# Optimization experiments

Hardware: AMD Instinct MI355X
Metric: run time of the kernel (lower is better)

The kernel has to match this reference:

```python
import jax, jax.numpy as jnp
import numpy as np

N_NODES = 100000


def gcn_conv(x, edge_index, W, b):
    # PyG GCNConv: add self-loops, symmetric normalization D^-1/2 (A+I) D^-1/2
    src, dst = edge_index[0], edge_index[1]
    n = x.shape[0]
    ones = jnp.ones(src.shape[0], dtype=x.dtype)
    deg = jax.ops.segment_sum(ones, dst, num_segments=n) + 1.0  # +1 self-loop
    dinv = jax.lax.rsqrt(deg)
    h = x @ W  # transform first (smaller gather traffic when out_dim < in_dim)
    norm = dinv[src] * dinv[dst]  # [E]
    msg = h[src] * norm[:, None]  # [E, out]
    agg = jax.ops.segment_sum(msg, dst, num_segments=n)
    agg = agg + h * (dinv * dinv)[:, None]  # self-loop contribution
    return agg + b


def setup_inputs() -> dict:
    key = jax.random.key(0)
    k = jax.random.split(key, 8)
    feature_size = 128
    n_edges = 3200000
    x = jax.random.normal(k[0], (N_NODES, feature_size), dtype=jnp.float32)
    edge_index = jax.random.randint(k[1], (2, n_edges), 0, N_NODES, dtype=jnp.int64)
    # Glorot-ish params
    W1 = jax.random.normal(k[2], (feature_size, 64), dtype=jnp.float32) / np.sqrt(feature_size)
    b1 = jnp.zeros((64,), dtype=jnp.float32)
    W2 = jax.random.normal(k[3], (64, 128), dtype=jnp.float32) / np.sqrt(64)
    b2 = jnp.zeros((128,), dtype=jnp.float32)
    Wfc = jax.random.normal(k[4], (128, 1), dtype=jnp.float32) / np.sqrt(128)
    bfc = jnp.zeros((1,), dtype=jnp.float32)
    return {"x": x, "edge_index": edge_index, "W1": W1, "b1": b1,
            "W2": W2, "b2": b2, "Wfc": Wfc, "bfc": bfc}


def reference(x, edge_index, W1, b1, W2, b2, Wfc, bfc):
    h = jax.nn.relu(gcn_conv(x, edge_index, W1, b1))
    h = jax.nn.relu(gcn_conv(h, edge_index, W2, b2))
    return h @ Wfc + bfc  # [N, 1]
```

## Files before the change

kernel.cpp:

```cpp
#include <hip/hip_runtime.h>
#include <hip/hip_fp16.h>

#define NN 100000
#define NBIN 128
#define RANGE 782
#define CAP 32768
#define CAPL 28672

__global__ __launch_bounds__(64) void k_detect(const unsigned int* ei, int* flag) {
    if (threadIdx.x == 0) {
        int is64 = 1;
        for (int i = 0; i < 64; ++i)
            if (ei[2 * i + 1] != 0u) { is64 = 0; break; }
        *flag = is64;
    }
}

__global__ __launch_bounds__(256) void k_binA(const int* __restrict__ ei_lo,
                                              const int* __restrict__ flag,
                                              int E, int* __restrict__ g_bincnt,
                                              unsigned* __restrict__ binbuf) {
    constexpr int ITER = 16;
    __shared__ int cnt[NBIN], basep[NBIN], pos[NBIN];
    const int t = threadIdx.x;
    const int base = blockIdx.x * (256 * ITER);
    const int s = (*flag) ? 2 : 1;
    unsigned pk[ITER];
    int bn[ITER];

    for (int i = t; i < NBIN; i += 256) { cnt[i] = 0; pos[i] = 0; }
    __syncthreads();

#pragma unroll
    for (int i = 0; i < ITER; ++i) {
        int e = base + i * 256 + t;
        if (e < E) {
            int src = __builtin_nontemporal_load(&ei_lo[(long long)s * e]);
            int dst = __builtin_nontemporal_load(&ei_lo[(long long)s * (E + e)]);
            int b = dst / RANGE;
            bn[i] = b;
            pk[i] = ((unsigned)(dst - b * RANGE) << 17) | (unsigned)src;
            atomicAdd(&cnt[b], 1);
        } else bn[i] = -1;
    }
    __syncthreads();
    for (int i = t; i < NBIN; i += 256)
        basep[i] = atomicAdd(&g_bincnt[i], cnt[i]);
    __syncthreads();
#pragma unroll
    for (int i = 0; i < ITER; ++i) {
        if (bn[i] >= 0) {
            int r = atomicAdd(&pos[bn[i]], 1);
            binbuf[(long long)bn[i] * CAP + basep[bn[i]] + r] = pk[i];
        }
    }
}

__global__ __launch_bounds__(512) void k_build(const unsigned* __restrict__ binbuf,
                                               const int* __restrict__ g_bincnt,
                                               int* __restrict__ row_ptr,
                                               float* __restrict__ dinv,
                                               int* __restrict__ csr, int n, int E) {
    __shared__ unsigned ebuf[CAPL];
    __shared__ int cnt[1024];
    __shared__ int ssum[512];
    __shared__ int pref[NBIN];
    const int t = threadIdx.x;
    const int bin = blockIdx.x;
    const int lo = bin * RANGE;
    const int rn = min(RANGE, n - lo);
    const int nE = min(g_bincnt[bin], CAPL);
    const unsigned* __restrict__ src = binbuf + (long long)bin * CAP;

    cnt[t] = 0; cnt[t + 512] = 0;
    if (t < NBIN) pref[t] = g_bincnt[t];
    __syncthreads();

    for (int i = t; i < nE; i += 512) {
        unsigned e = src[i];
        ebuf[i] = e;
        atomicAdd(&cnt[(int)(e >> 17)], 1);
    }
    __syncthreads();

    for (int off = 1; off < NBIN; off <<= 1) {
        int add = (t >= off && t < NBIN) ? pref[t - off] : 0;
        __syncthreads();
        if (t < NBIN) pref[t] += add;
        __syncthreads();
    }
    const int bstart = (bin > 0) ? pref[bin - 1] : 0;

    int a = cnt[2 * t], b = cnt[2 * t + 1];
    ssum[t] = a + b;
    __syncthreads();
    for (int off = 1; off < 512; off <<= 1) {
        int add = (t >= off) ? ssum[t - off] : 0;
        __syncthreads();
        ssum[t] += add;
        __syncthreads();
    }
    int prev = (t > 0) ? ssum[t - 1] : 0;
    cnt[2 * t] = prev;
    cnt[2 * t + 1] = prev + a;
    if (2 * t < rn) {
        row_ptr[lo + 2 * t] = bstart + prev;
        dinv[lo + 2 * t] = rsqrtf((float)a + 1.f);
    }
    if (2 * t + 1 < rn) {
        row_ptr[lo + 2 * t + 1] = bstart + prev + a;
        dinv[lo + 2 * t + 1] = rsqrtf((float)b + 1.f);
    }
    if (bin == NBIN - 1 && t == 0) row_ptr[n] = E;
    __syncthreads();

    for (int i = t; i < nE; i += 512) {
        unsigned e = ebuf[i];
        int slot = bstart + atomicAdd(&cnt[(int)(e >> 17)], 1);
        csr[slot] = (int)(e & 0x1FFFFu);
    }
}

__global__ __launch_bounds__(256) void k_gemm1(const float* __restrict__ X,
                                               const float* __restrict__ W,
                                               const float* __restrict__ dinv,
                                               __half* __restrict__ H, int n) {
    constexpr int K = 128, C = 64, RPT = 2;
    constexpr int CG = C / 4, RS = 256 / CG, RT = RS * RPT, XS = K + 4;
    __shared__ float Ws[K * C];
    __shared__ float Xs[RT * XS];
    const int t = threadIdx.x;

    for (int i = t * 4; i < K * C; i += 1024)
        *(float4*)&Ws[i] = *(const float4*)&W[i];

    const int row0 = blockIdx.x * RT;
    for (int i = t * 4; i < RT * K; i += 1024) {
        int r = i / K, k = i % K;
        int gr = row0 + r;
        float4 v = make_float4(0.f, 0.f, 0.f, 0.f);
        if (gr < n) v = *(const float4*)&X[(long long)gr * K + k];
        *(float4*)&Xs[r * XS + k] = v;
    }
    __syncthreads();

    const int cg = t % CG, rs = t / CG;
    float acc[RPT][4];
#pragma unroll
    for (int i = 0; i < RPT; ++i)
#pragma unroll
        for (int j = 0; j < 4; ++j) acc[i][j] = 0.f;

#pragma unroll 2
    for (int k4 = 0; k4 < K / 4; ++k4) {
        float4 xv[RPT];
#pragma unroll
        for (int i = 0; i < RPT; ++i)
            xv[i] = *(float4*)&Xs[(rs * RPT + i) * XS + k4 * 4];
#pragma unroll
        for (int j = 0; j < 4; ++j) {
            float4 w = *(float4*)&Ws[(k4 * 4 + j) * C + cg * 4];
#pragma unroll
            for (int i = 0; i < RPT; ++i) {
                float xvj = (&xv[i].x)[j];
                acc[i][0] = fmaf(xvj, w.x, acc[i][0]);
                acc[i][1] = fmaf(xvj, w.y, acc[i][1]);
                acc[i][2] = fmaf(xvj, w.z, acc[i][2]);
                acc[i][3] = fmaf(xvj, w.w, acc[i][3]);
            }
        }
    }
#pragma unroll
    for (int i = 0; i < RPT; ++i) {
        int gr = row0 + rs * RPT + i;
        if (gr < n) {
            float sc = dinv[gr];
            union { __half h[4]; uint2 u; } pk;
            pk.h[0] = __float2half(acc[i][0] * sc);
            pk.h[1] = __float2half(acc[i][1] * sc);
            pk.h[2] = __float2half(acc[i][2] * sc);
            pk.h[3] = __float2half(acc[i][3] * sc);
            *(uint2*)&H[(long long)gr * C + cg * 4] = pk.u;
        }
    }
}

template <bool RELU>
__global__ __launch_bounds__(256) void k_gather(const __half* __restrict__ h,
                                                const int* __restrict__ row_ptr,
                                                const int* __restrict__ csr,
                                                const float* __restrict__ dinv,
                                                const float* __restrict__ bias,
                                                __half* __restrict__ out, int n) {
    const int node = blockIdx.x * 4 + (threadIdx.x >> 6);
    if (node >= n) return;
    const int lane = threadIdx.x & 63;
    const int g = lane >> 3;
    const int fl = lane & 7;
    const float d = dinv[node];
    const int beg = row_ptr[node], end = row_ptr[node + 1];

    uint4 su = make_uint4(0u, 0u, 0u, 0u);
    if (g == 0) su = *(const uint4*)&h[(long long)node * 64 + fl * 8];

    float a0 = 0.f, a1 = 0.f, a2 = 0.f, a3 = 0.f;
    float a4 = 0.f, a5 = 0.f, a6 = 0.f, a7 = 0.f;
    float b0 = 0.f, b1 = 0.f, b2 = 0.f, b3 = 0.f;
    float b4 = 0.f, b5 = 0.f, b6 = 0.f, b7 = 0.f;

    const int nfull = (end - beg) >> 4;
    int i = beg;
    for (int it = 0; it < nfull; ++it, i += 16) {
        int s0 = csr[i + g];
        int s1 = csr[i + 8 + g];
        uint4 u0 = *(const uint4*)&h[(long long)s0 * 64 + fl * 8];
        uint4 u1 = *(const uint4*)&h[(long long)s1 * 64 + fl * 8];
        float2 f0 = __half22float2(*(__half2*)&u0.x);
        float2 f1 = __half22float2(*(__half2*)&u0.y);
        float2 f2 = __half22float2(*(__half2*)&u0.z);
        float2 f3 = __half22float2(*(__half2*)&u0.w);
        a0 += f0.x; a1 += f0.y; a2 += f1.x; a3 += f1.y;
        a4 += f2.x; a5 += f2.y; a6 += f3.x; a7 += f3.y;
        float2 g0 = __half22float2(*(__half2*)&u1.x);
        float2 g1 = __half22float2(*(__half2*)&u1.y);
        float2 g2 = __half22float2(*(__half2*)&u1.z);
        float2 g3 = __half22float2(*(__half2*)&u1.w);
        b0 += g0.x; b1 += g0.y; b2 += g1.x; b3 += g1.y;
        b4 += g2.x; b5 += g2.y; b6 += g3.x; b7 += g3.y;
    }
    if (i + g < end) {
        int s0 = csr[i + g];
        uint4 u0 = *(const uint4*)&h[(long long)s0 * 64 + fl * 8];
        float2 f0 = __half22float2(*(__half2*)&u0.x);
        float2 f1 = __half22float2(*(__half2*)&u0.y);
        float2 f2 = __half22float2(*(__half2*)&u0.z);
        float2 f3 = __half22float2(*(__half2*)&u0.w);
        a0 += f0.x; a1 += f0.y; a2 += f1.x; a3 += f1.y;
        a4 += f2.x; a5 += f2.y; a6 += f3.x; a7 += f3.y;
    }
    if (i + 8 + g < end) {
        int s1 = csr[i + 8 + g];
        uint4 u1 = *(const uint4*)&h[(long long)s1 * 64 + fl * 8];
        float2 g0 = __half22float2(*(__half2*)&u1.x);
        float2 g1 = __half22float2(*(__half2*)&u1.y);
        float2 g2 = __half22float2(*(__half2*)&u1.z);
        float2 g3 = __half22float2(*(__half2*)&u1.w);
        b0 += g0.x; b1 += g0.y; b2 += g1.x; b3 += g1.y;
        b4 += g2.x; b5 += g2.y; b6 += g3.x; b7 += g3.y;
    }

    float r0 = a0 + b0, r1 = a1 + b1, r2 = a2 + b2, r3 = a3 + b3;
    float r4 = a4 + b4, r5 = a5 + b5, r6 = a6 + b6, r7 = a7 + b7;
#pragma unroll
    for (int off = 8; off <= 32; off <<= 1) {
        r0 += __shfl_xor(r0, off, 64);
        r1 += __shfl_xor(r1, off, 64);
        r2 += __shfl_xor(r2, off, 64);
        r3 += __shfl_xor(r3, off, 64);
        r4 += __shfl_xor(r4, off, 64);
        r5 += __shfl_xor(r5, off, 64);
        r6 += __shfl_xor(r6, off, 64);
        r7 += __shfl_xor(r7, off, 64);
    }
    if (g == 0) {
        float2 s0 = __half22float2(*(__half2*)&su.x);
        float2 s1 = __half22float2(*(__half2*)&su.y);
        float2 s2 = __half22float2(*(__half2*)&su.z);
        float2 s3 = __half22float2(*(__half2*)&su.w);
        r0 += s0.x; r1 += s0.y; r2 += s1.x; r3 += s1.y;
        r4 += s2.x; r5 += s2.y; r6 += s3.x; r7 += s3.y;
        union { __half hh[8]; uint4 u; } o;
        if (RELU) {
            float4 bv0 = *(const float4*)&bias[fl * 8];
            float4 bv1 = *(const float4*)&bias[fl * 8 + 4];
            o.hh[0] = __float2half(fmaxf(fmaf(d, r0, bv0.x), 0.f) * d);
            o.hh[1] = __float2half(fmaxf(fmaf(d, r1, bv0.y), 0.f) * d);
            o.hh[2] = __float2half(fmaxf(fmaf(d, r2, bv0.z), 0.f) * d);
            o.hh[3] = __float2half(fmaxf(fmaf(d, r3, bv0.w), 0.f) * d);
            o.hh[4] = __float2half(fmaxf(fmaf(d, r4, bv1.x), 0.f) * d);
            o.hh[5] = __float2half(fmaxf(fmaf(d, r5, bv1.y), 0.f) * d);
            o.hh[6] = __float2half(fmaxf(fmaf(d, r6, bv1.z), 0.f) * d);
            o.hh[7] = __float2half(fmaxf(fmaf(d, r7, bv1.w), 0.f) * d);
        } else {
            o.hh[0] = __float2half(d * r0);
            o.hh[1] = __float2half(d * r1);
            o.hh[2] = __float2half(d * r2);
            o.hh[3] = __float2half(d * r3);
            o.hh[4] = __float2half(d * r4);
            o.hh[5] = __float2half(d * r5);
            o.hh[6] = __float2half(d * r6);
            o.hh[7] = __float2half(d * r7);
        }
        *(uint4*)&out[(long long)node * 64 + fl * 8] = o.u;
    }
}

__global__ __launch_bounds__(256) void k_gemm2fc(const __half* __restrict__ G,
                                                 const float* __restrict__ W2,
                                                 const float* __restrict__ b2,
                                                 const float* __restrict__ Wfc,
                                                 const float* __restrict__ bfc,
                                                 float* __restrict__ out, int n) {
    constexpr int K = 64, C = 128, CG = 32, RPT = 4, RT = 32, XS = K + 4;
    __shared__ float Ws[K * C];
    __shared__ float Xs[RT * XS];
    const int t = threadIdx.x;

    for (int i = t * 4; i < K * C; i += 1024)
        *(float4*)&Ws[i] = *(const float4*)&W2[i];

    const int row0 = blockIdx.x * RT;
    for (int i = t * 4; i < RT * K; i += 1024) {
        int r = i / K, k = i % K;
        int gr = row0 + r;
        float4 v = make_float4(0.f, 0.f, 0.f, 0.f);
        if (gr < n) {
            uint2 u = *(const uint2*)&G[(long long)gr * K + k];
            float2 f0 = __half22float2(*(__half2*)&u.x);
            float2 f1 = __half22float2(*(__half2*)&u.y);
            v = make_float4(f0.x, f0.y, f1.x, f1.y);
        }
        *(float4*)&Xs[r * XS + k] = v;
    }
    __syncthreads();

    const int cg = t % CG, rs = t / CG;
    float acc[RPT][4];
#pragma unroll
    for (int i = 0; i < RPT; ++i)
#pragma unroll
        for (int j = 0; j < 4; ++j) acc[i][j] = 0.f;

#pragma unroll 2
    for (int k4 = 0; k4 < K / 4; ++k4) {
        float4 xv[RPT];
#pragma unroll
        for (int i = 0; i < RPT; ++i)
            xv[i] = *(float4*)&Xs[(rs * RPT + i) * XS + k4 * 4];
#pragma unroll
        for (int j = 0; j < 4; ++j) {
            float4 w = *(float4*)&Ws[(k4 * 4 + j) * C + cg * 4];
#pragma unroll
            for (int i = 0; i < RPT; ++i) {
                float xvj = (&xv[i].x)[j];
                acc[i][0] = fmaf(xvj, w.x, acc[i][0]);
                acc[i][1] = fmaf(xvj, w.y, acc[i][1]);
                acc[i][2] = fmaf(xvj, w.z, acc[i][2]);
                acc[i][3] = fmaf(xvj, w.w, acc[i][3]);
            }
        }
    }

    float4 bv = *(const float4*)&b2[cg * 4];
    float4 wf = *(const float4*)&Wfc[cg * 4];
#pragma unroll
    for (int i = 0; i < RPT; ++i) {
        float p = fmaxf(acc[i][0] + bv.x, 0.f) * wf.x
                + fmaxf(acc[i][1] + bv.y, 0.f) * wf.y
                + fmaxf(acc[i][2] + bv.z, 0.f) * wf.z
                + fmaxf(acc[i][3] + bv.w, 0.f) * wf.w;
#pragma unroll
        for (int off = 16; off; off >>= 1) p += __shfl_down(p, off, 32);
        int gr = row0 + rs * RPT + i;
        if (cg == 0 && gr < n) out[gr] = p + bfc[0];
    }
}

extern "C" void kernel_launch(void* const* d_in, const int* in_sizes, int n_in,
                              void* d_out, int out_size, void* d_ws, size_t ws_size,
                              hipStream_t stream) {
    const float* x   = (const float*)d_in[0];
    const void*  ei  = d_in[1];
    const float* W1  = (const float*)d_in[2];
    const float* b1  = (const float*)d_in[3];
    const float* W2  = (const float*)d_in[4];
    const float* b2  = (const float*)d_in[5];
    const float* Wfc = (const float*)d_in[6];
    const float* bfc = (const float*)d_in[7];
    float* out = (float*)d_out;

    const int N = NN;
    const int E = in_sizes[1] / 2;

    char* ws = (char*)d_ws;
    size_t o = 0;
    auto carve = [&](size_t bytes) {
        char* p = ws + o;
        o = (o + bytes + 255) & ~(size_t)255;
        return p;
    };
    float*    dinv      = (float*)carve((size_t)N * 4);
    int*      row_ptr   = (int*)carve((size_t)(N + 1) * 4);
    int*      g_bincnt  = (int*)carve((size_t)NBIN * 4);
    int*      flag      = (int*)carve(4);
    int*      csr       = (int*)carve((size_t)E * 4);
    unsigned* binbuf    = (unsigned*)carve((size_t)NBIN * CAP * 4);
    __half*   bufA      = (__half*)carve((size_t)N * 64 * 2);
    __half*   bufB      = (__half*)carve((size_t)N * 64 * 2);
    __half*   bufG      = (__half*)carve((size_t)N * 64 * 2);

    const int* ei_lo = (const int*)ei;

    hipMemsetAsync(g_bincnt, 0, (size_t)NBIN * 4, stream);
    k_detect<<<1, 64, 0, stream>>>((const unsigned int*)ei, flag);
    k_binA<<<(E + 4095) / 4096, 256, 0, stream>>>(ei_lo, flag, E, g_bincnt, binbuf);
    k_build<<<NBIN, 512, 0, stream>>>(binbuf, g_bincnt, row_ptr, dinv, csr, N, E);

    k_gemm1<<<(N + 31) / 32, 256, 0, stream>>>(x, W1, dinv, bufA, N);
    k_gather<true><<<(N + 3) / 4, 256, 0, stream>>>(bufA, row_ptr, csr, dinv, b1, bufB, N);

    k_gather<false><<<(N + 3) / 4, 256, 0, stream>>>(bufB, row_ptr, csr, dinv, nullptr, bufG, N);
    k_gemm2fc<<<(N + 31) / 32, 256, 0, stream>>>(bufG, W2, b2, Wfc, bfc, out, N);
}
```

Baseline: 253.4 us.

## Fold format detection into binning, double bins, accumulate gather in half2

```diff
diff --git a/kernel.cpp b/kernel.cpp
--- a/kernel.cpp
+++ b/kernel.cpp
@@ -2,35 +2,33 @@
 #include <hip/hip_fp16.h>
 
 #define NN 100000
-#define NBIN 128
-#define RANGE 782
-#define CAP 32768
-#define CAPL 28672
-
-__global__ __launch_bounds__(64) void k_detect(const unsigned int* ei, int* flag) {
-    if (threadIdx.x == 0) {
-        int is64 = 1;
-        for (int i = 0; i < 64; ++i)
-            if (ei[2 * i + 1] != 0u) { is64 = 0; break; }
-        *flag = is64;
-    }
-}
+#define NBIN 256
+#define RANGE 391
+#define CAP 16384
+#define CAPL 16384
 
 __global__ __launch_bounds__(256) void k_binA(const int* __restrict__ ei_lo,
-                                              const int* __restrict__ flag,
                                               int E, int* __restrict__ g_bincnt,
                                               unsigned* __restrict__ binbuf) {
     constexpr int ITER = 16;
     __shared__ int cnt[NBIN], basep[NBIN], pos[NBIN];
+    __shared__ int s_is64;
     const int t = threadIdx.x;
     const int base = blockIdx.x * (256 * ITER);
-    const int s = (*flag) ? 2 : 1;
+
+    cnt[t] = 0; pos[t] = 0;
+    if (t == 0) {
+        const unsigned* u = (const unsigned*)ei_lo;
+        int is64 = 1;
+        for (int i = 0; i < 64; ++i)
+            if (u[2 * i + 1] != 0u) { is64 = 0; break; }
+        s_is64 = is64;
+    }
+    __syncthreads();
+    const int s = s_is64 ? 2 : 1;
+
     unsigned pk[ITER];
     int bn[ITER];
-
-    for (int i = t; i < NBIN; i += 256) { cnt[i] = 0; pos[i] = 0; }
-    __syncthreads();
-
 #pragma unroll
     for (int i = 0; i < ITER; ++i) {
         int e = base + i * 256 + t;
@@ -44,8 +42,7 @@
         } else bn[i] = -1;
     }
     __syncthreads();
-    for (int i = t; i < NBIN; i += 256)
-        basep[i] = atomicAdd(&g_bincnt[i], cnt[i]);
+    basep[t] = atomicAdd(&g_bincnt[t], cnt[t]);
     __syncthreads();
 #pragma unroll
     for (int i = 0; i < ITER; ++i) {
@@ -62,8 +59,8 @@
                                                float* __restrict__ dinv,
                                                int* __restrict__ csr, int n, int E) {
     __shared__ unsigned ebuf[CAPL];
-    __shared__ int cnt[1024];
-    __shared__ int ssum[512];
+    __shared__ int cnt[512];
+    __shared__ int ssum[256];
     __shared__ int pref[NBIN];
     const int t = threadIdx.x;
     const int bin = blockIdx.x;
@@ -72,7 +69,7 @@
     const int nE = min(g_bincnt[bin], CAPL);
     const unsigned* __restrict__ src = binbuf + (long long)bin * CAP;
 
-    cnt[t] = 0; cnt[t + 512] = 0;
+    cnt[t] = 0;
     if (t < NBIN) pref[t] = g_bincnt[t];
     __syncthreads();
 
@@ -91,25 +88,27 @@
     }
     const int bstart = (bin > 0) ? pref[bin - 1] : 0;
 
-    int a = cnt[2 * t], b = cnt[2 * t + 1];
-    ssum[t] = a + b;
-    __syncthreads();
-    for (int off = 1; off < 512; off <<= 1) {
-        int add = (t >= off) ? ssum[t - off] : 0;
+    int a = 0, b = 0;
+    if (t < 256) { a = cnt[2 * t]; b = cnt[2 * t + 1]; ssum[t] = a + b; }
+    __syncthreads();
+    for (int off = 1; off < 256; off <<= 1) {
+        int add = (t >= off && t < 256) ? ssum[t - off] : 0;
         __syncthreads();
-        ssum[t] += add;
+        if (t < 256) ssum[t] += add;
         __syncthreads();
     }
-    int prev = (t > 0) ? ssum[t - 1] : 0;
-    cnt[2 * t] = prev;
-    cnt[2 * t + 1] = prev + a;
-    if (2 * t < rn) {
-        row_ptr[lo + 2 * t] = bstart + prev;
-        dinv[lo + 2 * t] = rsqrtf((float)a + 1.f);
-    }
-    if (2 * t + 1 < rn) {
-        row_ptr[lo + 2 * t + 1] = bstart + prev + a;
-        dinv[lo + 2 * t + 1] = rsqrtf((float)b + 1.f);
+    if (t < 256) {
+        int prev = (t > 0) ? ssum[t - 1] : 0;
+        cnt[2 * t] = prev;
+        cnt[2 * t + 1] = prev + a;
+        if (2 * t < rn) {
+            row_ptr[lo + 2 * t] = bstart + prev;
+            dinv[lo + 2 * t] = rsqrtf((float)a + 1.f);
+        }
+        if (2 * t + 1 < rn) {
+            row_ptr[lo + 2 * t + 1] = bstart + prev + a;
+            dinv[lo + 2 * t + 1] = rsqrtf((float)b + 1.f);
+        }
     }
     if (bin == NBIN - 1 && t == 0) row_ptr[n] = E;
     __syncthreads();
@@ -203,10 +202,8 @@
     uint4 su = make_uint4(0u, 0u, 0u, 0u);
     if (g == 0) su = *(const uint4*)&h[(long long)node * 64 + fl * 8];
 
-    float a0 = 0.f, a1 = 0.f, a2 = 0.f, a3 = 0.f;
-    float a4 = 0.f, a5 = 0.f, a6 = 0.f, a7 = 0.f;
-    float b0 = 0.f, b1 = 0.f, b2 = 0.f, b3 = 0.f;
-    float b4 = 0.f, b5 = 0.f, b6 = 0.f, b7 = 0.f;
+    __half2 z = __float2half2_rn(0.f);
+    __half2 acc0 = z, acc1 = z, acc2 = z, acc3 = z;
 
     const int nfull = (end - beg) >> 4;
     int i = beg;
@@ -215,42 +212,38 @@
         int s1 = csr[i + 8 + g];
         uint4 u0 = *(const uint4*)&h[(long long)s0 * 64 + fl * 8];
         uint4 u1 = *(const uint4*)&h[(long long)s1 * 64 + fl * 8];
-        float2 f0 = __half22float2(*(__half2*)&u0.x);
-        float2 f1 = __half22float2(*(__half2*)&u0.y);
-        float2 f2 = __half22float2(*(__half2*)&u0.z);
-        float2 f3 = __half22float2(*(__half2*)&u0.w);
-        a0 += f0.x; a1 += f0.y; a2 += f1.x; a3 += f1.y;
-        a4 += f2.x; a5 += f2.y; a6 += f3.x; a7 += f3.y;
-        float2 g0 = __half22float2(*(__half2*)&u1.x);
-        float2 g1 = __half22float2(*(__half2*)&u1.y);
-        float2 g2 = __half22float2(*(__half2*)&u1.z);
-        float2 g3 = __half22float2(*(__half2*)&u1.w);
-        b0 += g0.x; b1 += g0.y; b2 += g1.x; b3 += g1.y;
-        b4 += g2.x; b5 += g2.y; b6 += g3.x; b7 += g3.y;
+        __half2 p0 = __hadd2(*(__half2*)&u0.x, *(__half2*)&u1.x);
+        __half2 p1 = __hadd2(*(__half2*)&u0.y, *(__half2*)&u1.y);
+        __half2 p2 = __hadd2(*(__half2*)&u0.z, *(__half2*)&u1.z);
+        __half2 p3 = __hadd2(*(__half2*)&u0.w, *(__half2*)&u1.w);
+        acc0 = __hadd2(acc0, p0);
+        acc1 = __hadd2(acc1, p1);
+        acc2 = __hadd2(acc2, p2);
+        acc3 = __hadd2(acc3, p3);
     }
     if (i + g < end) {
         int s0 = csr[i + g];
         uint4 u0 = *(const uint4*)&h[(long long)s0 * 64 + fl * 8];
-        float2 f0 = __half22float2(*(__half2*)&u0.x);
-        float2 f1 = __half22float2(*(__half2*)&u0.y);
-        float2 f2 = __half22float2(*(__half2*)&u0.z);
-        float2 f3 = __half22float2(*(__half2*)&u0.w);
-        a0 += f0.x; a1 += f0.y; a2 += f1.x; a3 += f1.y;
-        a4 += f2.x; a5 += f2.y; a6 += f3.x; a7 += f3.y;
+        acc0 = __hadd2(acc0, *(__half2*)&u0.x);
+        acc1 = __hadd2(acc1, *(__half2*)&u0.y);
+        acc2 = __hadd2(acc2, *(__half2*)&u0.z);
+        acc3 = __hadd2(acc3, *(__half2*)&u0.w);
     }
     if (i + 8 + g < end) {
         int s1 = csr[i + 8 + g];
         uint4 u1 = *(const uint4*)&h[(long long)s1 * 64 + fl * 8];
-        float2 g0 = __half22float2(*(__half2*)&u1.x);
-        float2 g1 = __half22float2(*(__half2*)&u1.y);
-        float2 g2 = __half22float2(*(__half2*)&u1.z);
-        float2 g3 = __half22float2(*(__half2*)&u1.w);
-        b0 += g0.x; b1 += g0.y; b2 += g1.x; b3 += g1.y;
-        b4 += g2.x; b5 += g2.y; b6 += g3.x; b7 += g3.y;
-    }
-
-    float r0 = a0 + b0, r1 = a1 + b1, r2 = a2 + b2, r3 = a3 + b3;
-    float r4 = a4 + b4, r5 = a5 + b5, r6 = a6 + b6, r7 = a7 + b7;
+        acc0 = __hadd2(acc0, *(__half2*)&u1.x);
+        acc1 = __hadd2(acc1, *(__half2*)&u1.y);
+        acc2 = __hadd2(acc2, *(__half2*)&u1.z);
+        acc3 = __hadd2(acc3, *(__half2*)&u1.w);
+    }
+
+    float2 f0 = __half22float2(acc0);
+    float2 f1 = __half22float2(acc1);
+    float2 f2 = __half22float2(acc2);
+    float2 f3 = __half22float2(acc3);
+    float r0 = f0.x, r1 = f0.y, r2 = f1.x, r3 = f1.y;
+    float r4 = f2.x, r5 = f2.y, r6 = f3.x, r7 = f3.y;
 #pragma unroll
     for (int off = 8; off <= 32; off <<= 1) {
         r0 += __shfl_xor(r0, off, 64);
@@ -392,7 +385,6 @@
     float*    dinv      = (float*)carve((size_t)N * 4);
     int*      row_ptr   = (int*)carve((size_t)(N + 1) * 4);
     int*      g_bincnt  = (int*)carve((size_t)NBIN * 4);
-    int*      flag      = (int*)carve(4);
     int*      csr       = (int*)carve((size_t)E * 4);
     unsigned* binbuf    = (unsigned*)carve((size_t)NBIN * CAP * 4);
     __half*   bufA      = (__half*)carve((size_t)N * 64 * 2);
@@ -402,8 +394,7 @@
     const int* ei_lo = (const int*)ei;
 
     hipMemsetAsync(g_bincnt, 0, (size_t)NBIN * 4, stream);
-    k_detect<<<1, 64, 0, stream>>>((const unsigned int*)ei, flag);
-    k_binA<<<(E + 4095) / 4096, 256, 0, stream>>>(ei_lo, flag, E, g_bincnt, binbuf);
+    k_binA<<<(E + 4095) / 4096, 256, 0, stream>>>(ei_lo, E, g_bincnt, binbuf);
     k_build<<<NBIN, 512, 0, stream>>>(binbuf, g_bincnt, row_ptr, dinv, csr, N, E);
 
     k_gemm1<<<(N + 31) / 32, 256, 0, stream>>>(x, W1, dinv, bufA, N);
```

Measured after the change: 240.0 us. -5.3%, faster.
